# Performance work log

Hardware: AMD Instinct MI355X
Metric: run time of the kernel (lower is better)

Reference implementation:

```python
import jax, jax.numpy as jnp
import numpy as np

B, T, S, A, U = 128, 512, 64, 8, 512  # batch, episode len, state dim, n_actions, n_units


def setup_inputs() -> dict:
    key = jax.random.key(0)
    ks = jax.random.split(key, 10)
    IN = S + A
    return {
        "states": jax.random.normal(ks[0], (B, T + 1, S), jnp.float32),
        "actions": jax.random.randint(ks[1], (B, T), 0, A),
        # cell-input gate: feedforward weights only, init N(0, 0.1)
        "W_ci": jax.random.normal(ks[2], (IN, U), jnp.float32) * 0.1,
        "b_ci": jax.random.normal(ks[3], (U,), jnp.float32),
        # input gate: recurrent weights only, init N(0, 0.1); bias mean -3
        "W_ig": jax.random.normal(ks[4], (U, U), jnp.float32) * 0.1,
        "b_ig": jax.random.normal(ks[5], (U,), jnp.float32) - 3.0,
        # output gate: feedforward weights only, init N(0, 0.1)
        "W_og": jax.random.normal(ks[6], (IN, U), jnp.float32) * 0.1,
        "b_og": jax.random.normal(ks[7], (U,), jnp.float32),
        # output head Linear(n_units, 1)
        "W_lin": jax.random.normal(ks[8], (U, 1), jnp.float32) * (1.0 / np.sqrt(U)),
        "b_lin": jnp.zeros((1,), jnp.float32),
    }


def reference(states, actions, W_ci, b_ci, W_ig, b_ig, W_og, b_og, W_lin, b_lin):
    Bv, T1, _ = states.shape
    # one-hot actions [B,T,A], pad one zero timestep -> [B,T+1,A]
    acts = jax.nn.one_hot(actions, A, dtype=states.dtype)
    acts = jnp.concatenate([acts, jnp.zeros((Bv, 1, A), states.dtype)], axis=1)
    x = jnp.concatenate([states, acts], axis=2)  # [B, T+1, S+A]

    # feedforward-only gates computed for all timesteps at once
    ci = jnp.tanh(jnp.einsum('bti,iu->btu', x, W_ci) + b_ci)          # cell input
    og = jax.nn.sigmoid(jnp.einsum('bti,iu->btu', x, W_og) + b_og)   # output gate

    def step(carry, inputs):
        c, h = carry
        ci_t, og_t = inputs
        ig = jax.nn.sigmoid(h @ W_ig + b_ig)  # recurrent-only input gate
        c = c + ci_t * ig                     # no forget gate: fg == 1
        h = c * og_t                          # a_out = identity
        return (c, h), h

    zeros = jnp.zeros((Bv, U), states.dtype)
    _, h_seq = jax.lax.scan(step, (zeros, zeros),
                            (jnp.swapaxes(ci, 0, 1), jnp.swapaxes(og, 0, 1)))
    h = jnp.swapaxes(h_seq, 0, 1)  # [B, T+1, U]
    return h @ W_lin + b_lin       # [B, T+1, 1]
```

## Files before the change

kernel.cpp:

```cpp
#include <hip/hip_runtime.h>
#include <cstdint>

#define NBATCH 128
#define NT 512
#define NT1 513
#define NS 64
#define NU 512
#define NBW 16
#define KF_SHORTS 16384
#define KF_V8 (KF_SHORTS / 8)
#define PACK_SHORTS (16 * KF_SHORTS)
#define CIOG_BYTES ((size_t)NT1 * NBATCH * NU * 4)
#define KF_AG 10
#define KF_VG 2
#define KF_LD 4
#define DYN_LDS (KF_LD * KF_SHORTS * 2)

typedef __attribute__((ext_vector_type(8))) short short8_t;
typedef __attribute__((ext_vector_type(4))) float f32x4;

__device__ __forceinline__ float sigf(float z) {
    return 1.0f / (1.0f + __expf(-z));
}
__device__ __forceinline__ float tanh_fast(float z) {
    return 2.0f / (1.0f + __expf(-2.0f * z)) - 1.0f;
}
__device__ __forceinline__ uint32_t bf16_top(float f) {
    uint32_t u = __float_as_uint(f);
    u += 0x7FFFu + ((u >> 16) & 1u);
    return u & 0xFFFF0000u;
}
__device__ __forceinline__ float f_from_lo(uint32_t p) { return __uint_as_float(p << 16); }
__device__ __forceinline__ float f_from_hi(uint32_t p) { return __uint_as_float(p & 0xFFFF0000u); }

__global__ __launch_bounds__(512) void pack_kernel(
    const float* __restrict__ W_ig, short* __restrict__ pack)
{
    const int g = blockIdx.x * 512 + threadIdx.x;
    const int lane = g & 63;
    const int nf = (g >> 6) & 3;
    const int wv = (g >> 8) & 7;
    const int kf = g >> 11;
    const int r16 = lane & 15, kg = lane >> 4;
    const int u = wv * 64 + nf * 16 + r16;
    const int kb = kf * 32 + kg * 8;
    short8_t w;
    #pragma unroll
    for (int j = 0; j < 8; ++j) {
        w[j] = (short)(bf16_top(W_ig[(size_t)(kb + j) * NU + u]) >> 16);
    }
    *(short8_t*)(pack + (size_t)g * 8) = w;
}

__global__ __launch_bounds__(512) void ff_kernel(
    const float* __restrict__ states, const int* __restrict__ actions,
    const float* __restrict__ W_ci, const float* __restrict__ b_ci,
    const float* __restrict__ W_og, const float* __restrict__ b_og,
    uint32_t* __restrict__ ciog)
{
    __shared__ __align__(16) float sh_s[32][64];
    __shared__ int sh_a[32];
    const int tid = threadIdx.x;
    const int b = blockIdx.x / 17;
    const int t0 = (blockIdx.x % 17) * 32;
    const int tcnt = (t0 + 32 <= NT1) ? 32 : (NT1 - t0);

    const float* sp = states + ((size_t)b * NT1 + t0) * NS;
    for (int j = tid; j < tcnt * 16; j += 512) {
        const float4 v = *(const float4*)(sp + j * 4);
        *(float4*)&sh_s[j >> 4][(j & 15) * 4] = v;
    }
    for (int tt = tid; tt < tcnt; tt += 512) {
        const int t = t0 + tt;
        sh_a[tt] = (t < NT) ? actions[b * NT + t] : -1;
    }
    __syncthreads();

    const int u = tid;
    float accc[32], acco[32];
    const float bc = b_ci[u], bo = b_og[u];
    #pragma unroll
    for (int tt = 0; tt < 32; ++tt) { accc[tt] = bc; acco[tt] = bo; }

    for (int i = 0; i < NS; ++i) {
        const float wc = W_ci[(size_t)i * NU + u];
        const float wo = W_og[(size_t)i * NU + u];
        #pragma unroll
        for (int tt = 0; tt < 32; ++tt) {
            const float s = sh_s[tt][i];
            accc[tt] = fmaf(s, wc, accc[tt]);
            acco[tt] = fmaf(s, wo, acco[tt]);
        }
    }
    #pragma unroll
    for (int tt = 0; tt < 32; ++tt) {
        if (tt < tcnt) {
            float zc = accc[tt], zo = acco[tt];
            const int a = sh_a[tt];
            if (a >= 0) {
                zc += W_ci[(size_t)(NS + a) * NU + u];
                zo += W_og[(size_t)(NS + a) * NU + u];
            }
            const float ci = tanh_fast(zc);
            const float og = sigf(zo);
            ciog[((size_t)(t0 + tt) * NBATCH + b) * NU + u] = bf16_top(og) | (bf16_top(ci) >> 16);
        }
    }
}

__global__ __attribute__((amdgpu_waves_per_eu(2, 2))) __launch_bounds__(512)
void rec_agpr2(
    const short* __restrict__ pack,
    const float* __restrict__ b_ig, const float* __restrict__ W_lin,
    const float* __restrict__ b_lin,
    const uint32_t* __restrict__ ciog,
    float* __restrict__ out)
{
    extern __shared__ __align__(16) char dynsm[];
    __shared__ __align__(16) short hsh[NBW * NU];
    __shared__ float ysum[2][8][NBW];

    const int tid  = threadIdx.x;
    const int lane = tid & 63;
    const int wv   = tid >> 6;
    const int n0   = wv << 6;
    const int r16  = lane & 15;
    const int kg   = lane >> 4;
    const int b0   = blockIdx.x * NBW;

    const short8_t* pr = (const short8_t*)pack;

    short8_t wag[KF_AG][4];
    #pragma unroll
    for (int kf = 0; kf < KF_AG; ++kf) {
        #pragma unroll
        for (int nf = 0; nf < 4; ++nf) {
            wag[kf][nf] = pr[((kf * 8 + wv) * 4 + nf) * 64 + lane];
            asm volatile("" : "+a"(wag[kf][nf]));
        }
    }
    short8_t wvg[KF_VG][4];
    #pragma unroll
    for (int kf = 0; kf < KF_VG; ++kf) {
        #pragma unroll
        for (int nf = 0; nf < 4; ++nf) {
            wvg[kf][nf] = pr[(((KF_AG + kf) * 8 + wv) * 4 + nf) * 64 + lane];
            asm volatile("" : "+v"(wvg[kf][nf]));
        }
    }

    short8_t* dl = (short8_t*)dynsm;
    {
        const short8_t* pl = pr + (KF_AG + KF_VG) * KF_V8;
        #pragma unroll
        for (int i = 0; i < 16; ++i) dl[i * 512 + tid] = pl[i * 512 + tid];
    }

    float big[4], wl[4];
    #pragma unroll
    for (int nf = 0; nf < 4; ++nf) {
        big[nf] = b_ig[n0 + nf * 16 + r16];
        wl[nf]  = W_lin[n0 + nf * 16 + r16];
    }
    const float blin = b_lin[0];

    for (int i = tid; i < NBW * NU; i += 512) hsh[i] = 0;

    float cst[4][4] = {{0.f,0.f,0.f,0.f},{0.f,0.f,0.f,0.f},
                       {0.f,0.f,0.f,0.f},{0.f,0.f,0.f,0.f}};

    const int amask = (r16 & 7) << 4;
    const char* hb = (const char*)hsh;
    char* hw = (char*)hsh;

    __syncthreads();

    for (int t = 0; t < NT1; ++t) {
        if (t > 0 && wv == 0 && lane < NBW) {
            float y = blin;
            #pragma unroll
            for (int w8 = 0; w8 < 8; ++w8) y += ysum[(t - 1) & 1][w8][lane];
            out[(size_t)(b0 + lane) * NT1 + (t - 1)] = y;
        }

        f32x4 acc[4];
        #pragma unroll
        for (int nf = 0; nf < 4; ++nf) { acc[nf][0]=0.f; acc[nf][1]=0.f; acc[nf][2]=0.f; acc[nf][3]=0.f; }

        #define AFRAG(KF) (*(const short8_t*)(hb + r16 * 1024 + ((((KF) * 64) + kg * 16) ^ amask)))
        #define MF4(KF, W) { const short8_t a_ = AFRAG(KF); \
            acc[0] = __builtin_amdgcn_mfma_f32_16x16x32_bf16(a_, (W)[0], acc[0], 0, 0, 0); \
            acc[1] = __builtin_amdgcn_mfma_f32_16x16x32_bf16(a_, (W)[1], acc[1], 0, 0, 0); \
            acc[2] = __builtin_amdgcn_mfma_f32_16x16x32_bf16(a_, (W)[2], acc[2], 0, 0, 0); \
            acc[3] = __builtin_amdgcn_mfma_f32_16x16x32_bf16(a_, (W)[3], acc[3], 0, 0, 0); }

        MF4(0, wag[0]) MF4(1, wag[1]) MF4(2, wag[2]) MF4(3, wag[3]) MF4(4, wag[4])
        MF4(5, wag[5]) MF4(6, wag[6]) MF4(7, wag[7]) MF4(8, wag[8]) MF4(9, wag[9])

        MF4(10, wvg[0])
        MF4(11, wvg[1])

        uint32_t pk[4][4];
        {
            const uint32_t* cg = ciog + (size_t)t * (NBATCH * NU);
            #pragma unroll
            for (int nf = 0; nf < 4; ++nf) {
                #pragma unroll
                for (int j = 0; j < 4; ++j)
                    pk[nf][j] = cg[(size_t)(b0 + kg * 4 + j) * NU + n0 + nf * 16 + r16];
            }
        }

        #pragma unroll
        for (int kf = 0; kf < KF_LD; ++kf) {
            short8_t wt[4];
            #pragma unroll
            for (int nf = 0; nf < 4; ++nf)
                wt[nf] = dl[((kf * 8 + wv) * 4 + nf) * 64 + lane];
            MF4(12 + kf, wt)
        }
        #undef MF4
        #undef AFRAG

        __syncthreads();

        float yp[4] = {0.f, 0.f, 0.f, 0.f};
        #pragma unroll
        for (int nf = 0; nf < 4; ++nf) {
            const int u2 = (n0 + nf * 16 + r16) * 2;
            #pragma unroll
            for (int j = 0; j < 4; ++j) {
                const int b = kg * 4 + j;
                const float z   = acc[nf][j] + big[nf];
                const float igv = sigf(z);
                const uint32_t p = pk[nf][j];
                cst[nf][j] = fmaf(f_from_lo(p), igv, cst[nf][j]);
                const float hv = cst[nf][j] * f_from_hi(p);
                yp[j] = fmaf(hv, wl[nf], yp[j]);
                const int wb = b * 1024 + (u2 ^ ((b & 7) << 4));
                *(short*)(hw + wb) = (short)(bf16_top(hv) >> 16);
            }
        }

        #pragma unroll
        for (int m = 1; m <= 8; m <<= 1) {
            yp[0] += __shfl_xor(yp[0], m);
            yp[1] += __shfl_xor(yp[1], m);
            yp[2] += __shfl_xor(yp[2], m);
            yp[3] += __shfl_xor(yp[3], m);
        }
        if (r16 == 0) {
            #pragma unroll
            for (int j = 0; j < 4; ++j) ysum[t & 1][wv][kg * 4 + j] = yp[j];
        }

        __syncthreads();
    }

    if (wv == 0 && lane < NBW) {
        float y = blin;
        #pragma unroll
        for (int w8 = 0; w8 < 8; ++w8) y += ysum[0][w8][lane];
        out[(size_t)(b0 + lane) * NT1 + NT] = y;
    }
}

__device__ __forceinline__ void fma4(float4& acc, const float4 w, const float s) {
    acc.x = fmaf(w.x, s, acc.x);
    acc.y = fmaf(w.y, s, acc.y);
    acc.z = fmaf(w.z, s, acc.z);
    acc.w = fmaf(w.w, s, acc.w);
}

__global__ __launch_bounds__(512) void rec_fallback(
    const float* __restrict__ states, const int* __restrict__ actions,
    const float* __restrict__ W_ci, const float* __restrict__ b_ci,
    const float* __restrict__ W_ig, const float* __restrict__ b_ig,
    const float* __restrict__ W_og, const float* __restrict__ b_og,
    const float* __restrict__ W_lin, const float* __restrict__ b_lin,
    float* __restrict__ out)
{
    __shared__ __align__(16) float h_lds[2][NU];
    __shared__ __align__(16) float part[4][2][NU];
    __shared__ float ysum[8][2];
    __shared__ float x_lds[2][NS];
    __shared__ int a_lds[2];

    const int tid = threadIdx.x;
    const int b0 = blockIdx.x * 2;
    const int uq = tid & 127;
    const int kq = tid >> 7;
    const int k0 = kq << 7;

    h_lds[0][tid] = 0.0f;
    h_lds[1][tid] = 0.0f;
    float c0 = 0.0f, c1 = 0.0f;
    const float wlin = W_lin[tid];
    const float big_ = b_ig[tid];
    const float blin = b_lin[0];
    const float bc = b_ci[tid], bo = b_og[tid];
    __syncthreads();

    for (int t = 0; t < NT1; ++t) {
        if (tid < 128) {
            const int bb = tid >> 6, i = tid & 63;
            x_lds[bb][i] = states[((size_t)(b0 + bb) * NT1 + t) * NS + i];
        } else if (tid < 130) {
            const int bb = tid - 128;
            a_lds[bb] = (t < NT) ? actions[(b0 + bb) * NT + t] : -1;
        }

        float4 a0 = make_float4(0.f, 0.f, 0.f, 0.f);
        float4 a1 = make_float4(0.f, 0.f, 0.f, 0.f);
        for (int kk = 0; kk < 128; kk += 4) {
            const int k = k0 + kk;
            const float4 h0v = *(const float4*)&h_lds[0][k];
            const float4 h1v = *(const float4*)&h_lds[1][k];
            const float* wr = W_ig + (size_t)k * NU + (uq << 2);
            const float4 w0 = *(const float4*)(wr);
            const float4 w1 = *(const float4*)(wr + NU);
            const float4 w2 = *(const float4*)(wr + 2 * NU);
            const float4 w3 = *(const float4*)(wr + 3 * NU);
            fma4(a0, w0, h0v.x); fma4(a1, w0, h1v.x);
            fma4(a0, w1, h0v.y); fma4(a1, w1, h1v.y);
            fma4(a0, w2, h0v.z); fma4(a1, w2, h1v.z);
            fma4(a0, w3, h0v.w); fma4(a1, w3, h1v.w);
        }
        *(float4*)&part[kq][0][uq << 2] = a0;
        *(float4*)&part[kq][1][uq << 2] = a1;
        __syncthreads();

        float z0 = big_, z1 = big_;
        #pragma unroll
        for (int q = 0; q < 4; ++q) { z0 += part[q][0][tid]; z1 += part[q][1][tid]; }

        float zc0 = bc, zo0 = bo, zc1 = bc, zo1 = bo;
        for (int i = 0; i < NS; ++i) {
            const float wc = W_ci[(size_t)i * NU + tid];
            const float wo = W_og[(size_t)i * NU + tid];
            const float s0v = x_lds[0][i];
            const float s1v = x_lds[1][i];
            zc0 = fmaf(s0v, wc, zc0); zo0 = fmaf(s0v, wo, zo0);
            zc1 = fmaf(s1v, wc, zc1); zo1 = fmaf(s1v, wo, zo1);
        }
        const int a0i = a_lds[0], a1i = a_lds[1];
        if (a0i >= 0) { zc0 += W_ci[(size_t)(NS + a0i) * NU + tid]; zo0 += W_og[(size_t)(NS + a0i) * NU + tid]; }
        if (a1i >= 0) { zc1 += W_ci[(size_t)(NS + a1i) * NU + tid]; zo1 += W_og[(size_t)(NS + a1i) * NU + tid]; }
        const float ci0 = tanh_fast(zc0), og0 = sigf(zo0);
        const float ci1 = tanh_fast(zc1), og1 = sigf(zo1);

        const float ig0 = sigf(z0), ig1 = sigf(z1);
        c0 = fmaf(ci0, ig0, c0);
        c1 = fmaf(ci1, ig1, c1);
        const float h0 = c0 * og0, h1 = c1 * og1;
        h_lds[0][tid] = h0;
        h_lds[1][tid] = h1;

        float y0 = h0 * wlin, y1 = h1 * wlin;
        #pragma unroll
        for (int off = 32; off > 0; off >>= 1) {
            y0 += __shfl_xor(y0, off);
            y1 += __shfl_xor(y1, off);
        }
        if ((tid & 63) == 0) { ysum[tid >> 6][0] = y0; ysum[tid >> 6][1] = y1; }
        __syncthreads();

        if (tid < 2) {
            float y = blin;
            #pragma unroll
            for (int w = 0; w < 8; ++w) y += ysum[w][tid];
            out[(size_t)(b0 + tid) * NT1 + t] = y;
        }
    }
}

extern "C" void kernel_launch(void* const* d_in, const int* in_sizes, int n_in,
                              void* d_out, int out_size, void* d_ws, size_t ws_size,
                              hipStream_t stream) {
    const float* states = (const float*)d_in[0];
    const int*   actions= (const int*)d_in[1];
    const float* W_ci = (const float*)d_in[2];
    const float* b_ci = (const float*)d_in[3];
    const float* W_ig = (const float*)d_in[4];
    const float* b_ig = (const float*)d_in[5];
    const float* W_og = (const float*)d_in[6];
    const float* b_og = (const float*)d_in[7];
    const float* W_lin= (const float*)d_in[8];
    const float* b_lin= (const float*)d_in[9];
    float* out = (float*)d_out;

    const size_t need = CIOG_BYTES + (size_t)PACK_SHORTS * 2;
    if (ws_size >= need) {
        uint32_t* ciog = (uint32_t*)d_ws;
        short* pack = (short*)((char*)d_ws + CIOG_BYTES);

        (void)hipFuncSetAttribute((const void*)rec_agpr2,
                                  hipFuncAttributeMaxDynamicSharedMemorySize, DYN_LDS);

        pack_kernel<<<dim3(64), dim3(512), 0, stream>>>(W_ig, pack);
        ff_kernel<<<dim3(NBATCH * 17), dim3(512), 0, stream>>>(
            states, actions, W_ci, b_ci, W_og, b_og, ciog);
        rec_agpr2<<<dim3(NBATCH / NBW), dim3(512), DYN_LDS, stream>>>(
            pack, b_ig, W_lin, b_lin, ciog, out);
    } else {
        rec_fallback<<<dim3(NBATCH / 2), dim3(512), 0, stream>>>(
            states, actions, W_ci, b_ci, W_ig, b_ig, W_og, b_og, W_lin, b_lin, out);
    }
}
```

Baseline: 3.676 ms.

## Use 4 waves of 128 units each and stream the remaining weight slices from L2

The recurrent kernel now runs 256 threads (4 waves), each wave owning 128 output units with 8 accumulator tiles. Each wave keeps 8 K-slices of the bf16 W_ig in AGPRs and 4 in LDS. The last 4 K-slices are reloaded from global memory every timestep and double-buffered so those loads overlap with the MFMAs. The goal is to get more MFMA work per A-fragment load and fewer waves per barrier. The cost is an extra global weight load on every step and lower occupancy (one wave per EU), which could lengthen the serial per-step latency.

```diff
diff --git a/kernel.cpp b/kernel.cpp
--- a/kernel.cpp
+++ b/kernel.cpp
@@ -11,8 +11,7 @@
 #define KF_V8 (KF_SHORTS / 8)
 #define PACK_SHORTS (16 * KF_SHORTS)
 #define CIOG_BYTES ((size_t)NT1 * NBATCH * NU * 4)
-#define KF_AG 10
-#define KF_VG 2
+#define KF_AG 8
 #define KF_LD 4
 #define DYN_LDS (KF_LD * KF_SHORTS * 2)
 
@@ -38,11 +37,11 @@
 {
     const int g = blockIdx.x * 512 + threadIdx.x;
     const int lane = g & 63;
-    const int nf = (g >> 6) & 3;
-    const int wv = (g >> 8) & 7;
+    const int nf = (g >> 6) & 7;
+    const int wv = (g >> 9) & 3;
     const int kf = g >> 11;
     const int r16 = lane & 15, kg = lane >> 4;
-    const int u = wv * 64 + nf * 16 + r16;
+    const int u = wv * 128 + nf * 16 + r16;
     const int kb = kf * 32 + kg * 8;
     short8_t w;
     #pragma unroll
@@ -108,8 +107,8 @@
     }
 }
 
-__global__ __attribute__((amdgpu_waves_per_eu(2, 2))) __launch_bounds__(512)
-void rec_agpr2(
+__global__ __attribute__((amdgpu_waves_per_eu(1, 1))) __launch_bounds__(256)
+void rec_reg2(
     const short* __restrict__ pack,
     const float* __restrict__ b_ig, const float* __restrict__ W_lin,
     const float* __restrict__ b_lin,
@@ -118,56 +117,52 @@
 {
     extern __shared__ __align__(16) char dynsm[];
     __shared__ __align__(16) short hsh[NBW * NU];
-    __shared__ float ysum[2][8][NBW];
+    __shared__ float ysum[2][4][NBW];
 
     const int tid  = threadIdx.x;
     const int lane = tid & 63;
     const int wv   = tid >> 6;
-    const int n0   = wv << 6;
+    const int n0   = wv << 7;
     const int r16  = lane & 15;
     const int kg   = lane >> 4;
     const int b0   = blockIdx.x * NBW;
 
     const short8_t* pr = (const short8_t*)pack;
-
-    short8_t wag[KF_AG][4];
+    #define PIDX(KF_, NF_) (((((KF_) * 4) + wv) * 8 + (NF_)) * 64 + lane)
+
+    short8_t wag[KF_AG][8];
     #pragma unroll
     for (int kf = 0; kf < KF_AG; ++kf) {
         #pragma unroll
-        for (int nf = 0; nf < 4; ++nf) {
-            wag[kf][nf] = pr[((kf * 8 + wv) * 4 + nf) * 64 + lane];
+        for (int nf = 0; nf < 8; ++nf) {
+            wag[kf][nf] = pr[PIDX(kf, nf)];
             asm volatile("" : "+a"(wag[kf][nf]));
-        }
-    }
-    short8_t wvg[KF_VG][4];
-    #pragma unroll
-    for (int kf = 0; kf < KF_VG; ++kf) {
-        #pragma unroll
-        for (int nf = 0; nf < 4; ++nf) {
-            wvg[kf][nf] = pr[(((KF_AG + kf) * 8 + wv) * 4 + nf) * 64 + lane];
-            asm volatile("" : "+v"(wvg[kf][nf]));
         }
     }
 
     short8_t* dl = (short8_t*)dynsm;
     {
-        const short8_t* pl = pr + (KF_AG + KF_VG) * KF_V8;
-        #pragma unroll
-        for (int i = 0; i < 16; ++i) dl[i * 512 + tid] = pl[i * 512 + tid];
-    }
-
-    float big[4], wl[4];
-    #pragma unroll
-    for (int nf = 0; nf < 4; ++nf) {
+        const short8_t* pl = pr + KF_AG * KF_V8;
+        #pragma unroll
+        for (int i = 0; i < 32; ++i) dl[i * 256 + tid] = pl[i * 256 + tid];
+    }
+
+    float big[8], wl[8];
+    #pragma unroll
+    for (int nf = 0; nf < 8; ++nf) {
         big[nf] = b_ig[n0 + nf * 16 + r16];
         wl[nf]  = W_lin[n0 + nf * 16 + r16];
     }
     const float blin = b_lin[0];
 
-    for (int i = tid; i < NBW * NU; i += 512) hsh[i] = 0;
-
-    float cst[4][4] = {{0.f,0.f,0.f,0.f},{0.f,0.f,0.f,0.f},
-                       {0.f,0.f,0.f,0.f},{0.f,0.f,0.f,0.f}};
+    for (int i = tid; i < NBW * NU; i += 256) hsh[i] = 0;
+
+    float cst[8][4];
+    #pragma unroll
+    for (int nf = 0; nf < 8; ++nf) {
+        #pragma unroll
+        for (int j = 0; j < 4; ++j) cst[nf][j] = 0.0f;
+    }
 
     const int amask = (r16 & 7) << 4;
     const char* hb = (const char*)hsh;
@@ -176,57 +171,74 @@
     __syncthreads();
 
     for (int t = 0; t < NT1; ++t) {
+        short8_t sA[8], sB[8];
+        #pragma unroll
+        for (int nf = 0; nf < 8; ++nf) sA[nf] = pr[PIDX(12, nf)];
+        #pragma unroll
+        for (int nf = 0; nf < 8; ++nf) sB[nf] = pr[PIDX(13, nf)];
+
         if (t > 0 && wv == 0 && lane < NBW) {
             float y = blin;
             #pragma unroll
-            for (int w8 = 0; w8 < 8; ++w8) y += ysum[(t - 1) & 1][w8][lane];
+            for (int w4 = 0; w4 < 4; ++w4) y += ysum[(t - 1) & 1][w4][lane];
             out[(size_t)(b0 + lane) * NT1 + (t - 1)] = y;
         }
 
-        f32x4 acc[4];
-        #pragma unroll
-        for (int nf = 0; nf < 4; ++nf) { acc[nf][0]=0.f; acc[nf][1]=0.f; acc[nf][2]=0.f; acc[nf][3]=0.f; }
+        f32x4 acc[8];
+        #pragma unroll
+        for (int nf = 0; nf < 8; ++nf) { acc[nf][0]=0.f; acc[nf][1]=0.f; acc[nf][2]=0.f; acc[nf][3]=0.f; }
 
         #define AFRAG(KF) (*(const short8_t*)(hb + r16 * 1024 + ((((KF) * 64) + kg * 16) ^ amask)))
-        #define MF4(KF, W) { const short8_t a_ = AFRAG(KF); \
+        #define MF8(KF, W) { const short8_t a_ = AFRAG(KF); \
             acc[0] = __builtin_amdgcn_mfma_f32_16x16x32_bf16(a_, (W)[0], acc[0], 0, 0, 0); \
             acc[1] = __builtin_amdgcn_mfma_f32_16x16x32_bf16(a_, (W)[1], acc[1], 0, 0, 0); \
             acc[2] = __builtin_amdgcn_mfma_f32_16x16x32_bf16(a_, (W)[2], acc[2], 0, 0, 0); \
-            acc[3] = __builtin_amdgcn_mfma_f32_16x16x32_bf16(a_, (W)[3], acc[3], 0, 0, 0); }
-
-        MF4(0, wag[0]) MF4(1, wag[1]) MF4(2, wag[2]) MF4(3, wag[3]) MF4(4, wag[4])
-        MF4(5, wag[5]) MF4(6, wag[6]) MF4(7, wag[7]) MF4(8, wag[8]) MF4(9, wag[9])
-
-        MF4(10, wvg[0])
-        MF4(11, wvg[1])
-
-        uint32_t pk[4][4];
+            acc[3] = __builtin_amdgcn_mfma_f32_16x16x32_bf16(a_, (W)[3], acc[3], 0, 0, 0); \
+            acc[4] = __builtin_amdgcn_mfma_f32_16x16x32_bf16(a_, (W)[4], acc[4], 0, 0, 0); \
+            acc[5] = __builtin_amdgcn_mfma_f32_16x16x32_bf16(a_, (W)[5], acc[5], 0, 0, 0); \
+            acc[6] = __builtin_amdgcn_mfma_f32_16x16x32_bf16(a_, (W)[6], acc[6], 0, 0, 0); \
+            acc[7] = __builtin_amdgcn_mfma_f32_16x16x32_bf16(a_, (W)[7], acc[7], 0, 0, 0); }
+
+        MF8(0, wag[0]) MF8(1, wag[1]) MF8(2, wag[2]) MF8(3, wag[3])
+        MF8(4, wag[4]) MF8(5, wag[5]) MF8(6, wag[6]) MF8(7, wag[7])
+
+        uint32_t pk[8][4];
         {
             const uint32_t* cg = ciog + (size_t)t * (NBATCH * NU);
             #pragma unroll
-            for (int nf = 0; nf < 4; ++nf) {
+            for (int nf = 0; nf < 8; ++nf) {
                 #pragma unroll
                 for (int j = 0; j < 4; ++j)
                     pk[nf][j] = cg[(size_t)(b0 + kg * 4 + j) * NU + n0 + nf * 16 + r16];
             }
         }
 
+        MF8(12, sA)
+        #pragma unroll
+        for (int nf = 0; nf < 8; ++nf) sA[nf] = pr[PIDX(14, nf)];
+        MF8(13, sB)
+        #pragma unroll
+        for (int nf = 0; nf < 8; ++nf) sB[nf] = pr[PIDX(15, nf)];
+
         #pragma unroll
         for (int kf = 0; kf < KF_LD; ++kf) {
-            short8_t wt[4];
-            #pragma unroll
-            for (int nf = 0; nf < 4; ++nf)
-                wt[nf] = dl[((kf * 8 + wv) * 4 + nf) * 64 + lane];
-            MF4(12 + kf, wt)
-        }
-        #undef MF4
+            short8_t wt[8];
+            #pragma unroll
+            for (int nf = 0; nf < 8; ++nf)
+                wt[nf] = dl[((kf * 4 + wv) * 8 + nf) * 64 + lane];
+            MF8(KF_AG + kf, wt)
+        }
+
+        MF8(14, sA)
+        MF8(15, sB)
+        #undef MF8
         #undef AFRAG
 
         __syncthreads();
 
         float yp[4] = {0.f, 0.f, 0.f, 0.f};
         #pragma unroll
-        for (int nf = 0; nf < 4; ++nf) {
+        for (int nf = 0; nf < 8; ++nf) {
             const int u2 = (n0 + nf * 16 + r16) * 2;
             #pragma unroll
             for (int j = 0; j < 4; ++j) {
@@ -260,9 +272,10 @@
     if (wv == 0 && lane < NBW) {
         float y = blin;
         #pragma unroll
-        for (int w8 = 0; w8 < 8; ++w8) y += ysum[0][w8][lane];
+        for (int w4 = 0; w4 < 4; ++w4) y += ysum[0][w4][lane];
         out[(size_t)(b0 + lane) * NT1 + NT] = y;
     }
+    #undef PIDX
 }
 
 __device__ __forceinline__ void fma4(float4& acc, const float4 w, const float s) {
@@ -394,13 +407,13 @@
         uint32_t* ciog = (uint32_t*)d_ws;
         short* pack = (short*)((char*)d_ws + CIOG_BYTES);
 
-        (void)hipFuncSetAttribute((const void*)rec_agpr2,
+        (void)hipFuncSetAttribute((const void*)rec_reg2,
                                   hipFuncAttributeMaxDynamicSharedMemorySize, DYN_LDS);
 
         pack_kernel<<<dim3(64), dim3(512), 0, stream>>>(W_ig, pack);
         ff_kernel<<<dim3(NBATCH * 17), dim3(512), 0, stream>>>(
             states, actions, W_ci, b_ci, W_og, b_og, ciog);
-        rec_agpr2<<<dim3(NBATCH / NBW), dim3(512), DYN_LDS, stream>>>(
+        rec_reg2<<<dim3(NBATCH / NBW), dim3(256), DYN_LDS, stream>>>(
             pack, b_ig, W_lin, b_lin, ciog, out);
     } else {
         rec_fallback<<<dim3(NBATCH / 2), dim3(512), 0, stream>>>(
```

After: 5.044 ms. 1.37x slower.

## Stream recurrent weight fragments from global memory via rotating register buffers

Applied to the files above, without the earlier changes.

Replaces the register-resident recurrent weights (10 fragments pinned in AGPRs, 2 in VGPRs) with a four-slot rotating register buffer. The buffer is refilled from the packed global weight array while MFMAs consume the previous slot. The waves_per_eu attribute is dropped, presumably to relieve register pressure and let the compiler schedule freely. The cost is re-reading the weights from cache every timestep, putting load latency on the sequential recurrence path.

```diff
diff --git a/kernel.cpp b/kernel.cpp
--- a/kernel.cpp
+++ b/kernel.cpp
@@ -11,8 +11,7 @@
 #define KF_V8 (KF_SHORTS / 8)
 #define PACK_SHORTS (16 * KF_SHORTS)
 #define CIOG_BYTES ((size_t)NT1 * NBATCH * NU * 4)
-#define KF_AG 10
-#define KF_VG 2
+#define KF_ST 12
 #define KF_LD 4
 #define DYN_LDS (KF_LD * KF_SHORTS * 2)
 
@@ -108,8 +107,7 @@
     }
 }
 
-__global__ __attribute__((amdgpu_waves_per_eu(2, 2))) __launch_bounds__(512)
-void rec_agpr2(
+__global__ __launch_bounds__(512) void rec_stream(
     const short* __restrict__ pack,
     const float* __restrict__ b_ig, const float* __restrict__ W_lin,
     const float* __restrict__ b_lin,
@@ -129,29 +127,13 @@
     const int b0   = blockIdx.x * NBW;
 
     const short8_t* pr = (const short8_t*)pack;
-
-    short8_t wag[KF_AG][4];
-    #pragma unroll
-    for (int kf = 0; kf < KF_AG; ++kf) {
-        #pragma unroll
-        for (int nf = 0; nf < 4; ++nf) {
-            wag[kf][nf] = pr[((kf * 8 + wv) * 4 + nf) * 64 + lane];
-            asm volatile("" : "+a"(wag[kf][nf]));
-        }
-    }
-    short8_t wvg[KF_VG][4];
-    #pragma unroll
-    for (int kf = 0; kf < KF_VG; ++kf) {
-        #pragma unroll
-        for (int nf = 0; nf < 4; ++nf) {
-            wvg[kf][nf] = pr[(((KF_AG + kf) * 8 + wv) * 4 + nf) * 64 + lane];
-            asm volatile("" : "+v"(wvg[kf][nf]));
-        }
-    }
+    #define PIDX(KF_, NF_) (((((KF_) * 8) + wv) * 4 + (NF_)) * 64 + lane)
+    #define LD4(S_, KF_) { (S_)[0] = pr[PIDX(KF_, 0)]; (S_)[1] = pr[PIDX(KF_, 1)]; \
+                           (S_)[2] = pr[PIDX(KF_, 2)]; (S_)[3] = pr[PIDX(KF_, 3)]; }
 
     short8_t* dl = (short8_t*)dynsm;
     {
-        const short8_t* pl = pr + (KF_AG + KF_VG) * KF_V8;
+        const short8_t* pl = pr + KF_ST * KF_V8;
         #pragma unroll
         for (int i = 0; i < 16; ++i) dl[i * 512 + tid] = pl[i * 512 + tid];
     }
@@ -172,6 +154,9 @@
     const int amask = (r16 & 7) << 4;
     const char* hb = (const char*)hsh;
     char* hw = (char*)hsh;
+
+    short8_t S0[4], S1[4], S2[4], S3[4];
+    LD4(S0, 0) LD4(S1, 1) LD4(S2, 2) LD4(S3, 3)
 
     __syncthreads();
 
@@ -194,11 +179,14 @@
             acc[2] = __builtin_amdgcn_mfma_f32_16x16x32_bf16(a_, (W)[2], acc[2], 0, 0, 0); \
             acc[3] = __builtin_amdgcn_mfma_f32_16x16x32_bf16(a_, (W)[3], acc[3], 0, 0, 0); }
 
-        MF4(0, wag[0]) MF4(1, wag[1]) MF4(2, wag[2]) MF4(3, wag[3]) MF4(4, wag[4])
-        MF4(5, wag[5]) MF4(6, wag[6]) MF4(7, wag[7]) MF4(8, wag[8]) MF4(9, wag[9])
-
-        MF4(10, wvg[0])
-        MF4(11, wvg[1])
+        MF4(0,  S0)  LD4(S0, 4)
+        MF4(1,  S1)  LD4(S1, 5)
+        MF4(2,  S2)  LD4(S2, 6)
+        MF4(3,  S3)  LD4(S3, 7)
+        MF4(4,  S0)  LD4(S0, 8)
+        MF4(5,  S1)  LD4(S1, 9)
+        MF4(6,  S2)  LD4(S2, 10)
+        MF4(7,  S3)  LD4(S3, 11)
 
         uint32_t pk[4][4];
         {
@@ -211,13 +199,18 @@
             }
         }
 
+        MF4(8,  S0)  LD4(S0, 0)
+        MF4(9,  S1)  LD4(S1, 1)
+        MF4(10, S2)  LD4(S2, 2)
+        MF4(11, S3)  LD4(S3, 3)
+
         #pragma unroll
         for (int kf = 0; kf < KF_LD; ++kf) {
             short8_t wt[4];
             #pragma unroll
             for (int nf = 0; nf < 4; ++nf)
                 wt[nf] = dl[((kf * 8 + wv) * 4 + nf) * 64 + lane];
-            MF4(12 + kf, wt)
+            MF4(KF_ST + kf, wt)
         }
         #undef MF4
         #undef AFRAG
@@ -263,6 +256,8 @@
         for (int w8 = 0; w8 < 8; ++w8) y += ysum[0][w8][lane];
         out[(size_t)(b0 + lane) * NT1 + NT] = y;
     }
+    #undef LD4
+    #undef PIDX
 }
 
 __device__ __forceinline__ void fma4(float4& acc, const float4 w, const float s) {
@@ -394,13 +389,13 @@
         uint32_t* ciog = (uint32_t*)d_ws;
         short* pack = (short*)((char*)d_ws + CIOG_BYTES);
 
-        (void)hipFuncSetAttribute((const void*)rec_agpr2,
+        (void)hipFuncSetAttribute((const void*)rec_stream,
                                   hipFuncAttributeMaxDynamicSharedMemorySize, DYN_LDS);
 
         pack_kernel<<<dim3(64), dim3(512), 0, stream>>>(W_ig, pack);
         ff_kernel<<<dim3(NBATCH * 17), dim3(512), 0, stream>>>(
             states, actions, W_ci, b_ci, W_og, b_og, ciog);
-        rec_agpr2<<<dim3(NBATCH / NBW), dim3(512), DYN_LDS, stream>>>(
+        rec_stream<<<dim3(NBATCH / NBW), dim3(512), DYN_LDS, stream>>>(
             pack, b_ig, W_lin, b_lin, ciog, out);
     } else {
         rec_fallback<<<dim3(NBATCH / 2), dim3(512), 0, stream>>>(
```

New measurement: 3.438 ms. 6.5% less time.
